# Kernel tuning notes

Hardware: AMD Instinct MI355X
Metric: run time of the kernel (lower is better)

## Reference

```python
import jax, jax.numpy as jnp
import numpy as np

B, E, S = 2, 1024, 2048
H = 16
D_QK = D_V = D_OUT = 1024
NEG = -1e4


def setup_inputs() -> dict:
    key = jax.random.key(0)
    ks = jax.random.split(key, 12)
    q = jax.random.normal(ks[0], (B, E, 1, S), jnp.float32)
    k = jax.random.normal(ks[1], (B, E, 1, S), jnp.float32)
    v = jax.random.normal(ks[2], (B, E, 1, S), jnp.float32)
    # causal qk_mask: (B, src, 1, tgt); src index > tgt index is masked
    causal = jnp.where(jnp.arange(S)[:, None] > jnp.arange(S)[None, :], NEG, 0.0).astype(jnp.float32)
    qk_mask = jnp.broadcast_to(causal[None, :, None, :], (B, S, 1, S))
    k_mask = jnp.zeros((B, S, 1, 1), jnp.float32)
    sc = 1.0 / np.sqrt(E)
    Wq = jax.random.normal(ks[3], (D_QK, E), jnp.float32) * sc
    Wk = jax.random.normal(ks[4], (D_QK, E), jnp.float32) * sc
    Wv = jax.random.normal(ks[5], (D_V, E), jnp.float32) * sc
    Wo = jax.random.normal(ks[6], (D_OUT, D_V), jnp.float32) * sc
    bq = jnp.zeros((D_QK,), jnp.float32)
    bk = jnp.zeros((D_QK,), jnp.float32)
    bv = jnp.zeros((D_V,), jnp.float32)
    bo = jnp.zeros((D_OUT,), jnp.float32)
    return {"q": q, "k": k, "v": v, "qk_mask": qk_mask, "k_mask": k_mask,
            "Wq": Wq, "bq": bq, "Wk": Wk, "bk": bk, "Wv": Wv, "bv": bv,
            "Wo": Wo, "bo": bo}


def reference(q, k, v, qk_mask, k_mask, Wq, bq, Wk, bk, Wv, bv, Wo, bo):
    b, _, _, tq = q.shape
    sk = k.shape[3]
    d_qk, d_v = Wq.shape[0], Wv.shape[0]
    dh, dvh = d_qk // H, d_v // H
    fact = float(dh) ** (-0.5)
    # 1x1 conv projections on (B, C, 1, S) == matmul over channels
    qp = jnp.einsum('oc,bcis->bois', Wq, q) + bq[None, :, None, None]
    kp = jnp.einsum('oc,bcis->bois', Wk, k) + bk[None, :, None, None]
    vp = jnp.einsum('oc,bcis->bois', Wv, v) + bv[None, :, None, None]
    # split heads: channel dim is head-major (contiguous chunks)
    qh = qp[:, :, 0, :].reshape(b, H, dh, tq)
    kh = kp[:, :, 0, :].reshape(b, H, dh, sk)
    vh = vp[:, :, 0, :].reshape(b, H, dvh, sk)
    # scores: (B, H, src, tgt); masks broadcast over heads
    scores = jnp.einsum('bhcq,bhck->bhkq', qh, kh) * fact
    scores = scores + qk_mask[:, None, :, 0, :] + k_mask[:, None, :, 0, 0][..., None]
    w = jax.nn.softmax(scores, axis=2)  # softmax over src (k) axis
    attn = jnp.einsum('bhkq,bhck->bhcq', w, vh).reshape(b, d_v, 1, tq)
    out = jnp.einsum('oc,bcis->bois', Wo, attn) + bo[None, :, None, None]
    return out
```

## Files before the change

### kernel.cpp

```cpp
#include <hip/hip_runtime.h>
#include <hip/hip_bf16.h>
#include <stdint.h>

typedef unsigned short u16;
typedef __attribute__((ext_vector_type(8))) short short8;
typedef __attribute__((ext_vector_type(4))) short short4v;
typedef __attribute__((ext_vector_type(4))) float f32x4;

#define MFMA16(a,b,c) __builtin_amdgcn_mfma_f32_16x16x32_bf16((a),(b),(c),0,0,0)
#define EXP2F(x) __builtin_amdgcn_exp2f(x)

typedef const __attribute__((address_space(1))) void glb_void;
typedef __attribute__((address_space(3))) void lds_void;

__device__ __forceinline__ u16 f2b(float f){
  unsigned u = __float_as_uint(f);
  u += 0x7fffu + ((u>>16)&1u);
  return (u16)(u>>16);
}
__device__ __forceinline__ unsigned pack_bf16(float a, float b){
  __hip_bfloat162 h = __float22bfloat162_rn(make_float2(a,b));
  unsigned u; __builtin_memcpy(&u, &h, 4); return u;
}
__device__ __forceinline__ void gld16(const void* g, void* l){
  __builtin_amdgcn_global_load_lds((glb_void*)g, (lds_void*)l, 16, 0, 0);
}

__device__ __forceinline__ const short8* frag64(const u16* lds, int row, int c16){
  return (const short8*)(lds + row*64 + ((c16 ^ (row&7))<<3));
}
__device__ __forceinline__ const short8* frag128(const u16* lds, int row, int c16){
  return (const short8*)(lds + row*128 + ((c16 ^ (row&15))<<3));
}

__global__ __launch_bounds__(256) void prep(
    const float* __restrict__ q, const float* __restrict__ k, const float* __restrict__ v,
    const float* __restrict__ qkm, const float* __restrict__ km,
    const float* __restrict__ Wq, const float* __restrict__ Wk,
    const float* __restrict__ Wv, const float* __restrict__ Wo,
    u16* __restrict__ W16, char* __restrict__ classes,
    u16* __restrict__ qT, u16* __restrict__ kT, u16* __restrict__ vT)
{
  __shared__ __align__(16) float t[64][72];
  const int bx = blockIdx.x, tid = threadIdx.x;
  const int S = 2048, E = 1024, nW = E*E;
  const float NEG = -1e4f;

  if (bx < 2048){
    const int sel = bx>>9, blk = bx&511;
    const float* src = sel==0?Wq : sel==1?Wk : sel==2?Wv : Wo;
    const float sc = (sel==0) ? 0.18033688f : 1.0f;
    u16* dst = W16 + (size_t)sel*nW;
    int i = (blk*256 + tid)*8;
    float4 a = *(const float4*)(src+i);
    float4 b = *(const float4*)(src+i+4);
    short8 o;
    o[0]=(short)f2b(a.x*sc); o[1]=(short)f2b(a.y*sc); o[2]=(short)f2b(a.z*sc); o[3]=(short)f2b(a.w*sc);
    o[4]=(short)f2b(b.x*sc); o[5]=(short)f2b(b.y*sc); o[6]=(short)f2b(b.z*sc); o[7]=(short)f2b(b.w*sc);
    *(short8*)(dst+i) = o;
  } else if (bx < 4096){
    const int tt = bx - 2048;
    const int b = tt>>10, qi = (tt>>5)&31, ki = tt&31;
    const int k0 = ki*64, q0 = qi*64;
    int az = 1, an = 1, ac = 1;
    #pragma unroll
    for (int p=0;p<4;++p){
      int e = tid + p*256;
      int row = e>>4, c4 = (e&15)*4;
      const int kg = k0 + row;
      float kmv = km[(size_t)b*S + kg];
      float4 mv = *(const float4*)&qkm[((size_t)b*S + kg)*S + q0 + c4];
      mv.x += kmv; mv.y += kmv; mv.z += kmv; mv.w += kmv;
      az &= (mv.x==0.f) & (mv.y==0.f) & (mv.z==0.f) & (mv.w==0.f);
      an &= (mv.x<-1e3f) & (mv.y<-1e3f) & (mv.z<-1e3f) & (mv.w<-1e3f);
      const float e0 = (kg > q0+c4+0) ? NEG : 0.f;
      const float e1 = (kg > q0+c4+1) ? NEG : 0.f;
      const float e2 = (kg > q0+c4+2) ? NEG : 0.f;
      const float e3 = (kg > q0+c4+3) ? NEG : 0.f;
      ac &= (mv.x==e0) & (mv.y==e1) & (mv.z==e2) & (mv.w==e3);
    }
    const int az_all = __syncthreads_and(az);
    const int an_all = __syncthreads_and(an);
    const int ac_all = __syncthreads_and(ac);
    if (tid==0)
      classes[((size_t)b*32 + qi)*32 + ki] =
          an_all ? 2 : (az_all ? 0 : (ac_all ? 3 : 1));
  } else {
    const int tt = bx - 4096;
    const int tensor = tt>>10, r = tt&1023;
    const int b = r>>9, rr = r&511;
    const int c0 = (rr>>5)*64, s0 = (rr&31)*64;
    const float* x = tensor==0 ? q : tensor==1 ? k : v;
    u16* xt = tensor==0 ? qT : tensor==1 ? kT : vT;
    #pragma unroll
    for (int p=0;p<4;++p){
      int e = tid + p*256;
      int row = e>>4, c4 = (e&15)*4;
      *(float4*)&t[row][c4] = *(const float4*)&x[((size_t)b*E + c0 + row)*S + s0 + c4];
    }
    __syncthreads();
    #pragma unroll
    for (int p=0;p<2;++p){
      int e = tid + p*256;
      int row = e>>3, col8 = (e&7)*8;
      short8 o;
      #pragma unroll
      for (int u=0;u<8;++u) o[u] = (short)f2b(t[col8+u][row]);
      *(short8*)&xt[((size_t)b*S + s0 + row)*E + c0 + col8] = o;
    }
  }
}

template<bool F32OUT>
__device__ __forceinline__ void gemm_core(
    const u16* __restrict__ A, const u16* __restrict__ Bt, const float* __restrict__ bias,
    float bscale, void* __restrict__ Cv, size_t cbase, int N, int K, int bias_on_m,
    int m0, int n0, u16* As, u16* Bs)
{
  const int tid = threadIdx.x, w = tid>>6, lane = tid&63;
  const int ln = lane&15, quad = lane>>4;
  const int m0w = (w>>1)*64, n0w = (w&1)*64;
  const int sub = lane>>3, gcol = ((lane&7)^sub)<<3;
  f32x4 acc[4][4];
  #pragma unroll
  for(int i=0;i<4;++i)
    #pragma unroll
    for(int j=0;j<4;++j) acc[i][j] = f32x4{0.f,0.f,0.f,0.f};

  short8 areg[4], breg[4];
  auto issue = [&](int kc){
    #pragma unroll
    for (int i=0;i<4;++i){
      const int r0 = (w*4+i)*8 + sub;
      areg[i] = *(const short8*)(A  + (size_t)(m0 + r0)*K + kc + gcol);
      breg[i] = *(const short8*)(Bt + (size_t)(n0 + r0)*K + kc + gcol);
    }
  };
  auto write_lds = [&](){
    #pragma unroll
    for (int i=0;i<4;++i){
      *(short8*)&As[(w*4+i)*512 + lane*8] = areg[i];
      *(short8*)&Bs[(w*4+i)*512 + lane*8] = breg[i];
    }
  };

  issue(0);
  for (int kc=0; kc<K; kc+=64){
    __builtin_amdgcn_s_barrier();
    __builtin_amdgcn_sched_barrier(0);
    write_lds();
    if (kc+64 < K) issue(kc+64);
    asm volatile("s_waitcnt lgkmcnt(0)" ::: "memory");
    __builtin_amdgcn_s_barrier();
    __builtin_amdgcn_sched_barrier(0);
    #pragma unroll
    for (int kk=0; kk<64; kk+=32){
      const int c16 = (kk>>3) + quad;
      short8 af[4], bf[4];
      #pragma unroll
      for (int mt=0;mt<4;++mt) af[mt] = *frag64(As, m0w+mt*16+ln, c16);
      #pragma unroll
      for (int nt=0;nt<4;++nt) bf[nt] = *frag64(Bs, n0w+nt*16+ln, c16);
      #pragma unroll
      for (int mt=0;mt<4;++mt)
        #pragma unroll
        for (int nt=0;nt<4;++nt)
          acc[mt][nt] = MFMA16(af[mt], bf[nt], acc[mt][nt]);
    }
  }
  #pragma unroll
  for (int mt=0;mt<4;++mt){
    #pragma unroll
    for (int nt=0;nt<4;++nt){
      const int col = n0 + n0w + nt*16 + ln;
      const float bn = bias_on_m ? 0.f : bias[col]*bscale;
      #pragma unroll
      for (int r=0;r<4;++r){
        const int row = m0 + m0w + mt*16 + quad*4 + r;
        const float bb = bias_on_m ? bias[row]*bscale : bn;
        const float val = acc[mt][nt][r] + bb;
        const size_t idx = cbase + (size_t)row*N + col;
        if (F32OUT) ((float*)Cv)[idx] = val;
        else        ((u16*)Cv)[idx]   = f2b(val);
      }
    }
  }
}

__global__ __launch_bounds__(256,2) void proj(
    const u16* __restrict__ qT, const u16* __restrict__ kT, const u16* __restrict__ vT,
    const u16* __restrict__ W16,
    const float* __restrict__ bq, const float* __restrict__ bk, const float* __restrict__ bv,
    u16* __restrict__ Qb, u16* __restrict__ Kb, u16* __restrict__ Vb)
{
  __shared__ __align__(16) u16 As[128*64];
  __shared__ __align__(16) u16 Bs[128*64];
  const int bx = blockIdx.x;
  const int zone = bx>>7, r = bx&127;
  const size_t sSE = (size_t)2048*1024;
  const int nW = 1024*1024;
  if (zone < 4){
    const int sel = zone>>1, b = zone&1;
    const int m0 = (r>>3)*128, n0 = (r&7)*128;
    gemm_core<false>((sel? kT : qT) + b*sSE, W16 + (size_t)sel*nW, sel? bk : bq,
                     sel? 1.0f : 0.18033688f, sel? Kb : Qb, b*sSE,
                     1024, 1024, 0, m0, n0, As, Bs);
  } else {
    const int b = zone&1;
    const int m0 = (r>>4)*128, n0 = (r&15)*128;
    gemm_core<false>(W16 + (size_t)2*nW, vT + b*sSE, bv,
                     1.0f, Vb, b*sSE,
                     2048, 1024, 1, m0, n0, As, Bs);
  }
}

__global__ __launch_bounds__(256,3) void gemm_out64(
    const u16* __restrict__ Wo16, const u16* __restrict__ At, const float* __restrict__ bo,
    float* __restrict__ out)
{
  __shared__ __align__(16) u16 As[64*64];
  __shared__ __align__(16) u16 Bs[128*64];
  const int b = blockIdx.z;
  const int m0 = blockIdx.y*64, n0 = blockIdx.x*128;
  const size_t sSE = (size_t)2048*1024;
  const int K = 1024, N = 2048;
  const u16* Bt = At + b*sSE;
  const int tid = threadIdx.x, w = tid>>6, lane = tid&63;
  const int ln = lane&15, quad = lane>>4;
  const int m0w = (w>>1)*32, n0w = (w&1)*64;
  const int sub = lane>>3, gcol = ((lane&7)^sub)<<3;
  f32x4 acc[2][4];
  #pragma unroll
  for(int i=0;i<2;++i)
    #pragma unroll
    for(int j=0;j<4;++j) acc[i][j] = f32x4{0.f,0.f,0.f,0.f};

  short8 areg[2], breg[4];
  auto issue = [&](int kc){
    #pragma unroll
    for (int i=0;i<2;++i){
      const int r0 = (w*2+i)*8 + sub;
      areg[i] = *(const short8*)(Wo16 + (size_t)(m0 + r0)*K + kc + gcol);
    }
    #pragma unroll
    for (int i=0;i<4;++i){
      const int r0 = (w*4+i)*8 + sub;
      breg[i] = *(const short8*)(Bt + (size_t)(n0 + r0)*K + kc + gcol);
    }
  };
  auto write_lds = [&](){
    #pragma unroll
    for (int i=0;i<2;++i)
      *(short8*)&As[(w*2+i)*512 + lane*8] = areg[i];
    #pragma unroll
    for (int i=0;i<4;++i)
      *(short8*)&Bs[(w*4+i)*512 + lane*8] = breg[i];
  };

  issue(0);
  for (int kc=0; kc<K; kc+=64){
    __builtin_amdgcn_s_barrier();
    __builtin_amdgcn_sched_barrier(0);
    write_lds();
    if (kc+64 < K) issue(kc+64);
    asm volatile("s_waitcnt lgkmcnt(0)" ::: "memory");
    __builtin_amdgcn_s_barrier();
    __builtin_amdgcn_sched_barrier(0);
    #pragma unroll
    for (int kk=0; kk<64; kk+=32){
      const int c16 = (kk>>3) + quad;
      short8 af[2], bf[4];
      #pragma unroll
      for (int mt=0;mt<2;++mt) af[mt] = *frag64(As, m0w+mt*16+ln, c16);
      #pragma unroll
      for (int nt=0;nt<4;++nt) bf[nt] = *frag64(Bs, n0w+nt*16+ln, c16);
      #pragma unroll
      for (int mt=0;mt<2;++mt)
        #pragma unroll
        for (int nt=0;nt<4;++nt)
          acc[mt][nt] = MFMA16(af[mt], bf[nt], acc[mt][nt]);
    }
  }
  #pragma unroll
  for (int mt=0;mt<2;++mt){
    #pragma unroll
    for (int nt=0;nt<4;++nt){
      const int col = n0 + n0w + nt*16 + ln;
      #pragma unroll
      for (int r=0;r<4;++r){
        const int row = m0 + m0w + mt*16 + quad*4 + r;
        out[b*sSE + (size_t)row*N + col] = acc[mt][nt][r] + bo[row];
      }
    }
  }
}

__global__ __launch_bounds__(256,2) void attn(
    const u16* __restrict__ Qb, const u16* __restrict__ Kb, const u16* __restrict__ Vb,
    const float* __restrict__ qk_mask, const float* __restrict__ k_mask,
    const char* __restrict__ classes, u16* __restrict__ Ot)
{
  __shared__ __align__(16) u16 Ks[128*64];
  __shared__ __align__(16) u16 Vs[64*128];
  __shared__ __align__(16) u16 Ps[4*16*128];
  const int bx = blockIdx.x;
  const int st = 31 - (bx>>5);
  const int bh = bx & 31;
  const int b = bh & 1, h = bh >> 1;
  const int tid = threadIdx.x, w = tid>>6, lane = tid&63;
  const int ln = lane&15, quad = lane>>4;
  const int S = 2048;
  const float LOG2E = 1.44269504f, C2 = 16.0f;

  const int qg = st*64 + w*16 + ln;
  short8 qf[2];
  #pragma unroll
  for (int kkI=0;kkI<2;++kkI)
    qf[kkI] = *(const short8*)&Qb[((size_t)b*S + qg)*1024 + h*64 + kkI*32 + quad*8];

  const char* cl = classes + ((size_t)b*32 + st)*32;
  unsigned mMe=0;
  #pragma unroll
  for (int kt=0;kt<16;++kt)
    if (!((cl[2*kt]==2) & (cl[2*kt+1]==2))) mMe |= 1u<<kt;

  float rs = 0.f;
  f32x4 acc[4];
  #pragma unroll
  for (int ct=0;ct<4;++ct) acc[ct] = f32x4{0.f,0.f,0.f,0.f};

  char* Pbase = (char*)(Ps + w*16*128) + ln*256;
  const int rsw = (ln&7)<<4;

  const u16* gK = Kb + ((size_t)b*S)*1024 + h*64;
  const u16* gV = Vb + ((size_t)b*1024 + h*64)*S;
  const int subK = lane>>3, cK = ((lane&7)^subK)<<3;
  const int subV = lane>>4, cV0 = lane&15;

  short8 kreg[4], vreg[4];
  auto issue = [&](int kt){
    const int k0 = kt*128;
    #pragma unroll
    for (int i=0;i<4;++i){
      const int r = (w*4+i)*8 + subK;
      kreg[i] = *(const short8*)(gK + (size_t)(k0 + r)*1024 + cK);
    }
    #pragma unroll
    for (int i=0;i<4;++i){
      const int row = (w*4+i)*4 + subV;
      vreg[i] = *(const short8*)(gV + (size_t)row*S + k0 + ((cV0 ^ (row&15))<<3));
    }
  };
  auto write_lds = [&](){
    #pragma unroll
    for (int i=0;i<4;++i)
      *(short8*)&Ks[(w*4+i)*512 + lane*8] = kreg[i];
    #pragma unroll
    for (int i=0;i<4;++i)
      *(short8*)&Vs[(w*4+i)*512 + lane*8] = vreg[i];
  };

  auto compute = [&](int kt){
    const char c0 = cl[2*kt], c1 = cl[2*kt+1];
    const bool nomask = (c0|c1)==0;
    const bool analytic = (c0!=1) & (c1!=1);
    const int k0 = kt*128;
    #pragma unroll
    for (int t=0;t<8;++t){
      f32x4 s = f32x4{0.f,0.f,0.f,0.f};
      #pragma unroll
      for (int kkI=0;kkI<2;++kkI)
        s = MFMA16(*frag64(Ks, t*16+ln, kkI*4 + quad), qf[kkI], s);
      float e[4];
      if (nomask){
        #pragma unroll
        for (int r=0;r<4;++r) e[r] = EXP2F(s[r] - C2);
      } else if (analytic){
        #pragma unroll
        for (int r=0;r<4;++r){
          const int kg = k0 + t*16 + quad*4 + r;
          e[r] = (kg <= qg) ? EXP2F(s[r] - C2) : 0.f;
        }
      } else {
        #pragma unroll
        for (int r=0;r<4;++r){
          const int kg = k0 + t*16 + quad*4 + r;
          const float m = qk_mask[((size_t)b*S + kg)*S + qg] + k_mask[(size_t)b*S + kg];
          e[r] = EXP2F(fmaf(m, LOG2E, s[r]) - C2);
        }
      }
      rs += (e[0]+e[1]) + (e[2]+e[3]);
      uint2 pp;
      pp.x = pack_bf16(e[0], e[1]);
      pp.y = pack_bf16(e[2], e[3]);
      *(uint2*)(Pbase + ((t*32 + quad*8) ^ rsw)) = pp;
    }
    #pragma unroll
    for (int c=0;c<4;++c){
      const short8 pf = *(const short8*)(Pbase + ((c*64 + quad*16) ^ rsw));
      __builtin_amdgcn_s_setprio(1);
      #pragma unroll
      for (int ct=0;ct<4;++ct)
        acc[ct] = MFMA16(*frag128(Vs, ct*16+ln, c*4 + quad), pf, acc[ct]);
      __builtin_amdgcn_s_setprio(0);
    }
  };

  int cur = mMe ? (__ffs(mMe)-1) : 16;
  if (cur < 16) issue(cur);
  while (cur < 16){
    const unsigned above = mMe & (0xfffffffeu << cur);
    const int nxt = above ? (__ffs(above)-1) : 16;
    __builtin_amdgcn_s_barrier();
    __builtin_amdgcn_sched_barrier(0);
    write_lds();
    if (nxt < 16) issue(nxt);
    asm volatile("s_waitcnt lgkmcnt(0)" ::: "memory");
    __builtin_amdgcn_s_barrier();
    __builtin_amdgcn_sched_barrier(0);
    compute(cur);
    cur = nxt;
  }

  rs += __shfl_xor(rs, 16, 64);
  rs += __shfl_xor(rs, 32, 64);
  const float rinv = 1.0f / rs;
  #pragma unroll
  for (int ct=0;ct<4;++ct){
    short4v o4;
    #pragma unroll
    for (int r=0;r<4;++r) o4[r] = (short)f2b(acc[ct][r] * rinv);
    *(short4v*)&Ot[((size_t)b*S + qg)*1024 + h*64 + ct*16 + quad*4] = o4;
  }
}

extern "C" void kernel_launch(void* const* d_in, const int* in_sizes, int n_in,
                              void* d_out, int out_size, void* d_ws, size_t ws_size,
                              hipStream_t stream)
{
  const float* q   = (const float*)d_in[0];
  const float* k   = (const float*)d_in[1];
  const float* v   = (const float*)d_in[2];
  const float* qkm = (const float*)d_in[3];
  const float* km  = (const float*)d_in[4];
  const float* Wq  = (const float*)d_in[5];
  const float* bq  = (const float*)d_in[6];
  const float* Wk  = (const float*)d_in[7];
  const float* bk  = (const float*)d_in[8];
  const float* Wv  = (const float*)d_in[9];
  const float* bv  = (const float*)d_in[10];
  const float* Wo  = (const float*)d_in[11];
  const float* bo  = (const float*)d_in[12];
  float* out = (float*)d_out;

  const size_t nAct = (size_t)2*2048*1024;
  const int   nW   = 1024*1024;

  u16* A0 = (u16*)d_ws;
  u16* A1 = A0 + nAct;
  u16* A2 = A1 + nAct;
  u16* A3 = A2 + nAct;
  u16* A4 = A3 + nAct;
  u16* A5 = A4 + nAct;
  u16* W16 = A5 + nAct;
  char* classes = (char*)(W16 + (size_t)4*nW);
  u16* Wo16 = W16 + (size_t)3*nW;

  dim3 blk(256);
  prep      <<<dim3(7168), blk, 0, stream>>>(q, k, v, qkm, km, Wq, Wk, Wv, Wo,
                                             W16, classes, A0, A1, A2);
  proj      <<<dim3(768),  blk, 0, stream>>>(A0, A1, A2, W16, bq, bk, bv, A3, A4, A5);
  attn      <<<dim3(1024), blk, 0, stream>>>(A3, A4, A5, qkm, km, classes, A0);
  gemm_out64<<<dim3(16,16,2), blk, 0, stream>>>(Wo16, A0, bo, out);
}
```

Baseline: 240.2 us.

## Split score computation by key rows across waves and skip fully masked halves

Each wave now computes scores for a 32-key slice against all 64 queries of the block, instead of all 128 keys against its own 16 queries. The P tile becomes block-shared, and a barrier is added between the score and PV phases. Halves whose class says fully masked (2) get zeroed P and skip their PV MFMAs. The row sum is now recomputed from the bf16 P values during PV, which costs extra conversion ALU work, an extra barrier per tile, and more Q fragment registers.

```diff
diff --git a/kernel.cpp b/kernel.cpp
--- a/kernel.cpp
+++ b/kernel.cpp
@@ -302,7 +302,7 @@
 {
   __shared__ __align__(16) u16 Ks[128*64];
   __shared__ __align__(16) u16 Vs[64*128];
-  __shared__ __align__(16) u16 Ps[4*16*128];
+  __shared__ __align__(16) u16 Ps[64*128];
   const int bx = blockIdx.x;
   const int st = 31 - (bx>>5);
   const int bh = bx & 31;
@@ -312,11 +312,13 @@
   const int S = 2048;
   const float LOG2E = 1.44269504f, C2 = 16.0f;
 
-  const int qg = st*64 + w*16 + ln;
-  short8 qf[2];
-  #pragma unroll
-  for (int kkI=0;kkI<2;++kkI)
-    qf[kkI] = *(const short8*)&Qb[((size_t)b*S + qg)*1024 + h*64 + kkI*32 + quad*8];
+  short8 qfg[4][2];
+  #pragma unroll
+  for (int g=0;g<4;++g)
+    #pragma unroll
+    for (int kkI=0;kkI<2;++kkI)
+      qfg[g][kkI] = *(const short8*)&Qb[((size_t)b*S + st*64 + g*16 + ln)*1024
+                                        + h*64 + kkI*32 + quad*8];
 
   const char* cl = classes + ((size_t)b*32 + st)*32;
   unsigned mMe=0;
@@ -329,8 +331,8 @@
   #pragma unroll
   for (int ct=0;ct<4;++ct) acc[ct] = f32x4{0.f,0.f,0.f,0.f};
 
-  char* Pbase = (char*)(Ps + w*16*128) + ln*256;
   const int rsw = (ln&7)<<4;
+  char* Pme = (char*)Ps + (w*16+ln)*256;
 
   const u16* gK = Kb + ((size_t)b*S)*1024 + h*64;
   const u16* gV = Vb + ((size_t)b*1024 + h*64)*S;
@@ -361,43 +363,70 @@
   };
 
   auto compute = [&](int kt){
-    const char c0 = cl[2*kt], c1 = cl[2*kt+1];
-    const bool nomask = (c0|c1)==0;
-    const bool analytic = (c0!=1) & (c1!=1);
+    const char chA = cl[2*kt], chB = cl[2*kt+1];
+    const char ch = (w>>1) ? chB : chA;
     const int k0 = kt*128;
-    #pragma unroll
-    for (int t=0;t<8;++t){
-      f32x4 s = f32x4{0.f,0.f,0.f,0.f};
-      #pragma unroll
-      for (int kkI=0;kkI<2;++kkI)
-        s = MFMA16(*frag64(Ks, t*16+ln, kkI*4 + quad), qf[kkI], s);
-      float e[4];
-      if (nomask){
+    if (ch == 2){
+      uint2 z; z.x = 0u; z.y = 0u;
+      #pragma unroll
+      for (int t=0;t<2;++t)
         #pragma unroll
-        for (int r=0;r<4;++r) e[r] = EXP2F(s[r] - C2);
-      } else if (analytic){
+        for (int g=0;g<4;++g)
+          *(uint2*)((char*)Ps + (g*16+ln)*256 + ((w*64 + t*32 + quad*8) ^ rsw)) = z;
+    } else {
+      const bool nomask = (ch==0);
+      const bool analytic = (ch==3);
+      #pragma unroll
+      for (int t=0;t<2;++t){
+        const int krow = w*32 + t*16 + ln;
+        const short8 af0 = *frag64(Ks, krow, quad);
+        const short8 af1 = *frag64(Ks, krow, 4 + quad);
         #pragma unroll
-        for (int r=0;r<4;++r){
-          const int kg = k0 + t*16 + quad*4 + r;
-          e[r] = (kg <= qg) ? EXP2F(s[r] - C2) : 0.f;
-        }
-      } else {
-        #pragma unroll
-        for (int r=0;r<4;++r){
-          const int kg = k0 + t*16 + quad*4 + r;
-          const float m = qk_mask[((size_t)b*S + kg)*S + qg] + k_mask[(size_t)b*S + kg];
-          e[r] = EXP2F(fmaf(m, LOG2E, s[r]) - C2);
+        for (int g=0;g<4;++g){
+          f32x4 s = f32x4{0.f,0.f,0.f,0.f};
+          s = MFMA16(af0, qfg[g][0], s);
+          s = MFMA16(af1, qfg[g][1], s);
+          const int qgg = st*64 + g*16 + ln;
+          float e[4];
+          if (nomask){
+            #pragma unroll
+            for (int r=0;r<4;++r) e[r] = EXP2F(s[r] - C2);
+          } else if (analytic){
+            #pragma unroll
+            for (int r=0;r<4;++r){
+              const int kg = k0 + w*32 + t*16 + quad*4 + r;
+              e[r] = (kg <= qgg) ? EXP2F(s[r] - C2) : 0.f;
+            }
+          } else {
+            #pragma unroll
+            for (int r=0;r<4;++r){
+              const int kg = k0 + w*32 + t*16 + quad*4 + r;
+              const float m = qk_mask[((size_t)b*S + kg)*S + qgg] + k_mask[(size_t)b*S + kg];
+              e[r] = EXP2F(fmaf(m, LOG2E, s[r]) - C2);
+            }
+          }
+          uint2 pp;
+          pp.x = pack_bf16(e[0], e[1]);
+          pp.y = pack_bf16(e[2], e[3]);
+          *(uint2*)((char*)Ps + (g*16+ln)*256 + ((w*64 + t*32 + quad*8) ^ rsw)) = pp;
         }
       }
-      rs += (e[0]+e[1]) + (e[2]+e[3]);
-      uint2 pp;
-      pp.x = pack_bf16(e[0], e[1]);
-      pp.y = pack_bf16(e[2], e[3]);
-      *(uint2*)(Pbase + ((t*32 + quad*8) ^ rsw)) = pp;
-    }
+    }
+    asm volatile("s_waitcnt lgkmcnt(0)" ::: "memory");
+    __builtin_amdgcn_s_barrier();
+    __builtin_amdgcn_sched_barrier(0);
     #pragma unroll
     for (int c=0;c<4;++c){
-      const short8 pf = *(const short8*)(Pbase + ((c*64 + quad*16) ^ rsw));
+      const char chc = (c>>1) ? chB : chA;
+      if (chc == 2) continue;
+      const short8 pf = *(const short8*)(Pme + ((c*64 + quad*16) ^ rsw));
+      #pragma unroll
+      for (int i=0;i<4;++i){
+        unsigned u = ((const unsigned*)&pf)[i];
+        __hip_bfloat162 h2; __builtin_memcpy(&h2, &u, 4);
+        float2 f2 = __bfloat1622float2(h2);
+        rs += f2.x + f2.y;
+      }
       __builtin_amdgcn_s_setprio(1);
       #pragma unroll
       for (int ct=0;ct<4;++ct)
@@ -425,6 +454,7 @@
   rs += __shfl_xor(rs, 16, 64);
   rs += __shfl_xor(rs, 32, 64);
   const float rinv = 1.0f / rs;
+  const int qg = st*64 + w*16 + ln;
   #pragma unroll
   for (int ct=0;ct<4;++ct){
     short4v o4;
```

After: 246.7 us. 2.7% more time.
